# Kernel optimization log

Measured on AMD Instinct MI355X. Metric: run time of the kernel, lower is better.

The kernel has to match this reference:

```python
import jax, jax.numpy as jnp
import numpy as np


def setup_inputs() -> dict:
    key = jax.random.key(0)
    k1, k2 = jax.random.split(key)
    B, S, D = 8, 2048, 1024
    x = jax.random.normal(k1, (B, S, D), dtype=jnp.float32)
    # xavier_uniform init for [D, D]
    limit = float(np.sqrt(6.0 / (D + D)))
    att_weight = jax.random.uniform(k2, (D, D), dtype=jnp.float32, minval=-limit, maxval=limit)
    bias = jnp.zeros((D,), dtype=jnp.float32)
    return {"x": x, "att_weight": att_weight, "bias": bias}


def reference(x, att_weight, bias):
    # Q = x @ W; K = V = x
    q = jnp.einsum("bsd,de->bse", x, att_weight)
    scale = 1.0 / jnp.sqrt(jnp.asarray(x.shape[-1], dtype=jnp.float32))
    scores = jnp.einsum("bqd,bkd->bqk", q, x) * scale  # [B,S,S]
    attn = jax.nn.softmax(scores, axis=-1)
    out = jnp.einsum("bqk,bkd->bqd", attn, x)
    return out + bias[None, None, :]
```

## Files before the change

kernel.cpp:

```cpp
#include <hip/hip_runtime.h>

typedef unsigned short u16;
typedef unsigned int u32;
typedef __attribute__((ext_vector_type(8))) short short8;
typedef __attribute__((ext_vector_type(4))) float floatx4;

__device__ __forceinline__ u16 f2bf(float f) {
  u32 u = __float_as_uint(f);
  u32 r = u + 0x7fffu + ((u >> 16) & 1u);
  return (u16)(r >> 16);
}

__device__ __forceinline__ void gload_lds16(const u16* g, u16* l) {
  __builtin_amdgcn_global_load_lds(
      (const __attribute__((address_space(1))) u32*)g,
      (__attribute__((address_space(3))) u32*)l, 16, 0, 0);
}

__global__ __launch_bounds__(256)
void cast_tr(const float* __restrict__ in, u16* __restrict__ cast_out,
             u16* __restrict__ tr_out, int rows, int cols, float scale,
             long bstride)
{
  __shared__ u16 tile[64][65];
  const int b = blockIdx.z;
  in += (long)b * bstride;
  if (cast_out) cast_out += (long)b * bstride;
  tr_out += (long)b * bstride;
  const int r0 = blockIdx.y * 64, c0 = blockIdx.x * 64;
  const int tx = threadIdx.x & 63, ty = threadIdx.x >> 6;

  for (int i = ty; i < 64; i += 4) {
    float v = in[(long)(r0 + i) * cols + c0 + tx] * scale;
    u16 h = f2bf(v);
    if (cast_out) cast_out[(long)(r0 + i) * cols + c0 + tx] = h;
    tile[i][tx] = h;
  }
  __syncthreads();
  for (int i = ty; i < 64; i += 4)
    tr_out[(long)(c0 + i) * rows + r0 + tx] = tile[tx][i];
}

#define BM 128
#define BN 128
#define BK 64

template<bool BF16_OUT>
__global__ __launch_bounds__(256, 3)
void gemm_nt(const u16* __restrict__ A, const u16* __restrict__ Bt,
             void* __restrict__ Cout, const float* __restrict__ bias,
             int M, int N, int K, int lda, int ldb, int ldc,
             long sA, long sB, long sC)
{
  __shared__ __align__(16) u16 As[BM * BK];
  __shared__ __align__(16) u16 Bs[BN * BK];

  const int bz = blockIdx.z;
  A  += (long)bz * sA;
  Bt += (long)bz * sB;

  const int tid  = threadIdx.x;
  const int wave = tid >> 6;
  const int lane = tid & 63;

  const int tileM = blockIdx.y * BM;
  const int tileN = blockIdx.x * BN;

  const int srow = lane >> 3;
  const int sj   = lane & 7;
  const int sjj  = sj ^ srow;

  const int wm = (wave >> 1) * 64;
  const int wn = (wave & 1) * 64;
  const int lc = lane & 15;
  const int lq = lane >> 4;

  floatx4 acc[4][4];
  #pragma unroll
  for (int i = 0; i < 4; ++i)
    #pragma unroll
    for (int j = 0; j < 4; ++j)
      acc[i][j] = (floatx4){0.f, 0.f, 0.f, 0.f};

  for (int k0 = 0; k0 < K; k0 += BK) {
    #pragma unroll
    for (int s = 0; s < 4; ++s) {
      const int rb = wave * 32 + s * 8;
      gload_lds16(A  + (long)(tileM + rb + srow) * lda + k0 + sjj * 8,
                  &As[rb * BK]);
      gload_lds16(Bt + (long)(tileN + rb + srow) * ldb + k0 + sjj * 8,
                  &Bs[rb * BK]);
    }
    __syncthreads();

    #pragma unroll
    for (int kk = 0; kk < BK; kk += 32) {
      const int jcb = (kk >> 3) + lq;
      short8 af[4], bf[4];
      #pragma unroll
      for (int i = 0; i < 4; ++i) {
        const int m = wm + i * 16 + lc;
        af[i] = *(const short8*)&As[m * BK + ((jcb ^ (m & 7)) << 3)];
      }
      #pragma unroll
      for (int j = 0; j < 4; ++j) {
        const int n = wn + j * 16 + lc;
        bf[j] = *(const short8*)&Bs[n * BK + ((jcb ^ (n & 7)) << 3)];
      }
      #pragma unroll
      for (int i = 0; i < 4; ++i)
        #pragma unroll
        for (int j = 0; j < 4; ++j)
          acc[i][j] = __builtin_amdgcn_mfma_f32_16x16x32_bf16(
                          af[i], bf[j], acc[i][j], 0, 0, 0);
    }
    __syncthreads();
  }

  if (BF16_OUT) {
    u16* C = (u16*)Cout + (long)bz * sC;
    #pragma unroll
    for (int i = 0; i < 4; ++i) {
      const int rb = tileM + wm + i * 16 + lq * 4;
      #pragma unroll
      for (int j = 0; j < 4; ++j) {
        const int col = tileN + wn + j * 16 + lc;
        #pragma unroll
        for (int r = 0; r < 4; ++r)
          C[(long)(rb + r) * ldc + col] = f2bf(acc[i][j][r]);
      }
    }
  } else {
    float* C = (float*)Cout + (long)bz * sC;
    #pragma unroll
    for (int i = 0; i < 4; ++i) {
      const int rb = tileM + wm + i * 16 + lq * 4;
      #pragma unroll
      for (int j = 0; j < 4; ++j) {
        const int col = tileN + wn + j * 16 + lc;
        const float bv = bias ? bias[col] : 0.f;
        #pragma unroll
        for (int r = 0; r < 4; ++r)
          C[(long)(rb + r) * ldc + col] = acc[i][j][r] + bv;
      }
    }
  }
}

__global__ __launch_bounds__(256)
void softmax_rows(u16* __restrict__ S, int ncol)
{
  __shared__ float redmax[4];
  __shared__ float redsum[4];
  const long row = blockIdx.x;
  u16* p = S + row * (long)ncol;
  const int t = threadIdx.x;
  const int lane = t & 63, wave = t >> 6;

  uint4 raw = ((const uint4*)p)[t];
  float v[8];
  v[0] = __uint_as_float(raw.x << 16); v[1] = __uint_as_float(raw.x & 0xffff0000u);
  v[2] = __uint_as_float(raw.y << 16); v[3] = __uint_as_float(raw.y & 0xffff0000u);
  v[4] = __uint_as_float(raw.z << 16); v[5] = __uint_as_float(raw.z & 0xffff0000u);
  v[6] = __uint_as_float(raw.w << 16); v[7] = __uint_as_float(raw.w & 0xffff0000u);

  float m = v[0];
  #pragma unroll
  for (int i = 1; i < 8; ++i) m = fmaxf(m, v[i]);
  #pragma unroll
  for (int off = 32; off > 0; off >>= 1) m = fmaxf(m, __shfl_xor(m, off, 64));
  if (lane == 0) redmax[wave] = m;
  __syncthreads();
  m = fmaxf(fmaxf(redmax[0], redmax[1]), fmaxf(redmax[2], redmax[3]));

  float s = 0.f;
  #pragma unroll
  for (int i = 0; i < 8; ++i) { v[i] = __expf(v[i] - m); s += v[i]; }
  #pragma unroll
  for (int off = 32; off > 0; off >>= 1) s += __shfl_xor(s, off, 64);
  if (lane == 0) redsum[wave] = s;
  __syncthreads();
  s = redsum[0] + redsum[1] + redsum[2] + redsum[3];
  const float inv = 1.0f / s;

  uint4 o;
  o.x = (u32)f2bf(v[0]*inv) | ((u32)f2bf(v[1]*inv) << 16);
  o.y = (u32)f2bf(v[2]*inv) | ((u32)f2bf(v[3]*inv) << 16);
  o.z = (u32)f2bf(v[4]*inv) | ((u32)f2bf(v[5]*inv) << 16);
  o.w = (u32)f2bf(v[6]*inv) | ((u32)f2bf(v[7]*inv) << 16);
  ((uint4*)p)[t] = o;
}

extern "C" void kernel_launch(void* const* d_in, const int* in_sizes, int n_in,
                              void* d_out, int out_size, void* d_ws, size_t ws_size,
                              hipStream_t stream) {
  const float* x    = (const float*)d_in[0];
  const float* W    = (const float*)d_in[1];
  const float* bias = (const float*)d_in[2];
  float* out        = (float*)d_out;
  (void)in_sizes; (void)n_in; (void)out_size; (void)ws_size;

  const int B = 8, S = 2048, D = 1024;
  const long BSD = (long)B * S * D;

  u16* Xb  = (u16*)d_ws;
  u16* XbT = Xb  + BSD;
  u16* Qb  = XbT + BSD;
  u16* Wt  = Qb  + BSD;
  u16* Sc  = Wt  + (long)D * D;

  dim3 blk(256);

  cast_tr<<<dim3(D/64, S/64, B), blk, 0, stream>>>(x, Xb, XbT, S, D, 1.0f, (long)S*D);
  cast_tr<<<dim3(D/64, D/64, 1), blk, 0, stream>>>(W, nullptr, Wt, D, D, 0.03125f, 0);

  gemm_nt<true><<<dim3(D/128, (B*S)/128, 1), blk, 0, stream>>>(
      Xb, Wt, Qb, nullptr, B*S, D, D, D, D, D, 0, 0, 0);

  gemm_nt<true><<<dim3(S/128, S/128, B), blk, 0, stream>>>(
      Qb, Xb, Sc, nullptr, S, S, D, D, D, S,
      (long)S*D, (long)S*D, (long)S*S);

  softmax_rows<<<dim3(B*S), blk, 0, stream>>>(Sc, S);

  gemm_nt<false><<<dim3(D/128, S/128, B), blk, 0, stream>>>(
      Sc, XbT, out, bias, S, D, S, S, S, D,
      (long)S*S, (long)D*S, (long)S*D);
}
```

Baseline: 362.8 us.

## Fuse exp and row-sum into score GEMM, normalize in output GEMM

Removes the separate softmax kernel. The score GEMM epilogue now applies exp, stores unnormalized bf16 probabilities and atomically adds per-row partial sums into a zeroed buffer. The final GEMM divides by the row sum before adding the bias. The max subtraction is dropped, so this relies on scores staying small enough not to overflow exp. It also adds grouped tile-order swizzling for L2 reuse across all GEMMs.

```diff
diff --git a/kernel.cpp b/kernel.cpp
--- a/kernel.cpp
+++ b/kernel.cpp
@@ -45,10 +45,11 @@
 #define BN 128
 #define BK 64
 
-template<bool BF16_OUT>
+template<int MODE>
 __global__ __launch_bounds__(256, 3)
 void gemm_nt(const u16* __restrict__ A, const u16* __restrict__ Bt,
              void* __restrict__ Cout, const float* __restrict__ bias,
+             float* __restrict__ rsum,
              int M, int N, int K, int lda, int ldb, int ldc,
              long sA, long sB, long sC)
 {
@@ -63,8 +64,16 @@
   const int wave = tid >> 6;
   const int lane = tid & 63;
 
-  const int tileM = blockIdx.y * BM;
-  const int tileN = blockIdx.x * BN;
+  const int nbx = gridDim.x, nby = gridDim.y;
+  const int pid  = blockIdx.y * nbx + blockIdx.x;
+  const int band = 8 * nbx;
+  const int gid  = pid / band;
+  const int fm   = gid * 8;
+  const int gsz  = min(nby - fm, 8);
+  const int pm   = fm + (pid % band) % gsz;
+  const int pn   = (pid % band) / gsz;
+  const int tileM = pm * BM;
+  const int tileN = pn * BN;
 
   const int srow = lane >> 3;
   const int sj   = lane & 7;
@@ -117,7 +126,7 @@
     __syncthreads();
   }
 
-  if (BF16_OUT) {
+  if (MODE == 0) {
     u16* C = (u16*)Cout + (long)bz * sC;
     #pragma unroll
     for (int i = 0; i < 4; ++i) {
@@ -130,65 +139,52 @@
           C[(long)(rb + r) * ldc + col] = f2bf(acc[i][j][r]);
       }
     }
+  } else if (MODE == 1) {
+    u16* C = (u16*)Cout + (long)bz * sC;
+    float* rs = rsum + (long)bz * M;
+    #pragma unroll
+    for (int i = 0; i < 4; ++i) {
+      const int rb = tileM + wm + i * 16 + lq * 4;
+      float rpart[4] = {0.f, 0.f, 0.f, 0.f};
+      #pragma unroll
+      for (int j = 0; j < 4; ++j) {
+        const int col = tileN + wn + j * 16 + lc;
+        #pragma unroll
+        for (int r = 0; r < 4; ++r) {
+          float e = __expf(acc[i][j][r]);
+          C[(long)(rb + r) * ldc + col] = f2bf(e);
+          rpart[r] += e;
+        }
+      }
+      #pragma unroll
+      for (int r = 0; r < 4; ++r) {
+        float s = rpart[r];
+        s += __shfl_xor(s, 1, 64);
+        s += __shfl_xor(s, 2, 64);
+        s += __shfl_xor(s, 4, 64);
+        s += __shfl_xor(s, 8, 64);
+        if (lc == 0) atomicAdd(&rs[rb + r], s);
+      }
+    }
   } else {
     float* C = (float*)Cout + (long)bz * sC;
+    const float* rs = rsum + (long)bz * M;
     #pragma unroll
     for (int i = 0; i < 4; ++i) {
       const int rb = tileM + wm + i * 16 + lq * 4;
+      float inv[4];
+      #pragma unroll
+      for (int r = 0; r < 4; ++r) inv[r] = 1.0f / rs[rb + r];
       #pragma unroll
       for (int j = 0; j < 4; ++j) {
         const int col = tileN + wn + j * 16 + lc;
-        const float bv = bias ? bias[col] : 0.f;
+        const float bv = bias[col];
         #pragma unroll
         for (int r = 0; r < 4; ++r)
-          C[(long)(rb + r) * ldc + col] = acc[i][j][r] + bv;
+          C[(long)(rb + r) * ldc + col] = acc[i][j][r] * inv[r] + bv;
       }
     }
   }
-}
-
-__global__ __launch_bounds__(256)
-void softmax_rows(u16* __restrict__ S, int ncol)
-{
-  __shared__ float redmax[4];
-  __shared__ float redsum[4];
-  const long row = blockIdx.x;
-  u16* p = S + row * (long)ncol;
-  const int t = threadIdx.x;
-  const int lane = t & 63, wave = t >> 6;
-
-  uint4 raw = ((const uint4*)p)[t];
-  float v[8];
-  v[0] = __uint_as_float(raw.x << 16); v[1] = __uint_as_float(raw.x & 0xffff0000u);
-  v[2] = __uint_as_float(raw.y << 16); v[3] = __uint_as_float(raw.y & 0xffff0000u);
-  v[4] = __uint_as_float(raw.z << 16); v[5] = __uint_as_float(raw.z & 0xffff0000u);
-  v[6] = __uint_as_float(raw.w << 16); v[7] = __uint_as_float(raw.w & 0xffff0000u);
-
-  float m = v[0];
-  #pragma unroll
-  for (int i = 1; i < 8; ++i) m = fmaxf(m, v[i]);
-  #pragma unroll
-  for (int off = 32; off > 0; off >>= 1) m = fmaxf(m, __shfl_xor(m, off, 64));
-  if (lane == 0) redmax[wave] = m;
-  __syncthreads();
-  m = fmaxf(fmaxf(redmax[0], redmax[1]), fmaxf(redmax[2], redmax[3]));
-
-  float s = 0.f;
-  #pragma unroll
-  for (int i = 0; i < 8; ++i) { v[i] = __expf(v[i] - m); s += v[i]; }
-  #pragma unroll
-  for (int off = 32; off > 0; off >>= 1) s += __shfl_xor(s, off, 64);
-  if (lane == 0) redsum[wave] = s;
-  __syncthreads();
-  s = redsum[0] + redsum[1] + redsum[2] + redsum[3];
-  const float inv = 1.0f / s;
-
-  uint4 o;
-  o.x = (u32)f2bf(v[0]*inv) | ((u32)f2bf(v[1]*inv) << 16);
-  o.y = (u32)f2bf(v[2]*inv) | ((u32)f2bf(v[3]*inv) << 16);
-  o.z = (u32)f2bf(v[4]*inv) | ((u32)f2bf(v[5]*inv) << 16);
-  o.w = (u32)f2bf(v[6]*inv) | ((u32)f2bf(v[7]*inv) << 16);
-  ((uint4*)p)[t] = o;
 }
 
 extern "C" void kernel_launch(void* const* d_in, const int* in_sizes, int n_in,
@@ -208,22 +204,23 @@
   u16* Qb  = XbT + BSD;
   u16* Wt  = Qb  + BSD;
   u16* Sc  = Wt  + (long)D * D;
+  float* rsum = (float*)(Sc + (long)B * S * S);
 
   dim3 blk(256);
+
+  hipMemsetAsync(rsum, 0, (size_t)B * S * sizeof(float), stream);
 
   cast_tr<<<dim3(D/64, S/64, B), blk, 0, stream>>>(x, Xb, XbT, S, D, 1.0f, (long)S*D);
   cast_tr<<<dim3(D/64, D/64, 1), blk, 0, stream>>>(W, nullptr, Wt, D, D, 0.03125f, 0);
 
-  gemm_nt<true><<<dim3(D/128, (B*S)/128, 1), blk, 0, stream>>>(
-      Xb, Wt, Qb, nullptr, B*S, D, D, D, D, D, 0, 0, 0);
-
-  gemm_nt<true><<<dim3(S/128, S/128, B), blk, 0, stream>>>(
-      Qb, Xb, Sc, nullptr, S, S, D, D, D, S,
+  gemm_nt<0><<<dim3(D/128, (B*S)/128, 1), blk, 0, stream>>>(
+      Xb, Wt, Qb, nullptr, nullptr, B*S, D, D, D, D, D, 0, 0, 0);
+
+  gemm_nt<1><<<dim3(S/128, S/128, B), blk, 0, stream>>>(
+      Qb, Xb, Sc, nullptr, rsum, S, S, D, D, D, S,
       (long)S*D, (long)S*D, (long)S*S);
 
-  softmax_rows<<<dim3(B*S), blk, 0, stream>>>(Sc, S);
-
-  gemm_nt<false><<<dim3(D/128, S/128, B), blk, 0, stream>>>(
-      Sc, XbT, out, bias, S, D, S, S, S, D,
+  gemm_nt<2><<<dim3(D/128, S/128, B), blk, 0, stream>>>(
+      Sc, XbT, out, bias, rsum, S, D, S, S, S, D,
       (long)S*S, (long)D*S, (long)S*D);
 }
```

Result: faster. 310.8 us (-14.3%).
